# Performance work log

Measured on AMD Instinct MI355X. Metric: run time of the kernel, lower is better.

Reference implementation:

```python
import jax, jax.numpy as jnp
import numpy as np

N, E, IN, H1, H2, C = 50000, 800000, 256, 64, 64, 40
NEG_SLOPE = 0.2


def _glorot(key, shape):
    fan_in = shape[0]
    return jax.random.normal(key, shape, jnp.float32) / np.sqrt(fan_in)


def gat_conv(x, W, al, ar, src, dst, act):
    """DGL-style GATConv (no bias, no residual). al/ar: [H, D]."""
    n = x.shape[0]
    H, D = al.shape
    feat = (x @ W).reshape(n, H, D)                      # [N,H,D]
    el = jnp.sum(feat * al, axis=-1)                     # [N,H]
    er = jnp.sum(feat * ar, axis=-1)                     # [N,H]
    e = jax.nn.leaky_relu(el[src] + er[dst], NEG_SLOPE)  # [E,H]
    # edge softmax over incoming edges of each dst node
    emax = jax.ops.segment_max(e, dst, num_segments=n)
    emax = jnp.where(jnp.isfinite(emax), emax, 0.0)      # guard zero-in-degree
    ex = jnp.exp(e - emax[dst])
    den = jax.ops.segment_sum(ex, dst, num_segments=n)
    alpha = ex / jnp.maximum(den[dst], 1e-9)             # [E,H]
    msg = feat[src] * alpha[..., None]                   # [E,H,D]
    rst = jax.ops.segment_sum(msg, dst, num_segments=n)  # [N,H,D]
    return act(rst) if act is not None else rst


def setup_inputs() -> dict:
    key = jax.random.key(0)
    ks = jax.random.split(key, 24)
    x = jax.random.normal(ks[0], (N, IN), jnp.float32)
    src = jax.random.randint(ks[1], (E,), 0, N, jnp.int32)
    dst = jax.random.randint(ks[2], (E,), 0, N, jnp.int32)
    p = {
        # branch 0 (even): GAT(num_layers=2, heads=[4,1,1])
        "W00": _glorot(ks[3], (IN, 4 * H1)),  "a00l": _glorot(ks[4], (4, H1)),  "a00r": _glorot(ks[5], (4, H1)),
        "W01": _glorot(ks[6], (4 * H1, H1)),  "a01l": _glorot(ks[7], (1, H1)),  "a01r": _glorot(ks[8], (1, H1)),
        "W0f": _glorot(ks[9], (H1, C)),       "a0fl": _glorot(ks[10], (1, C)),  "a0fr": _glorot(ks[11], (1, C)),
        # branch 1 (odd): GAT(num_layers=1, heads=[4,1]) encoder + 1-head output conv
        "W10": _glorot(ks[12], (IN, 4 * H2)), "a10l": _glorot(ks[13], (4, H2)), "a10r": _glorot(ks[14], (4, H2)),
        "W1f": _glorot(ks[15], (4 * H2, H1)), "a1fl": _glorot(ks[16], (1, H1)), "a1fr": _glorot(ks[17], (1, H1)),
        "W1o": _glorot(ks[18], (H1, C)),      "a1ol": _glorot(ks[19], (1, C)),  "a1or": _glorot(ks[20], (1, C)),
    }
    return {"x": x, "src": src, "dst": dst, **p}


def reference(x, src, dst,
              W00, a00l, a00r, W01, a01l, a01r, W0f, a0fl, a0fr,
              W10, a10l, a10r, W1f, a1fl, a1fr, W1o, a1ol, a1or):
    elu = jax.nn.elu
    n = x.shape[0]
    # branch 0: stacked GAT, final layer mean over heads, no activation
    h = gat_conv(x, W00, a00l, a00r, src, dst, elu).reshape(n, -1)   # [N,4*H1]
    h = gat_conv(h, W01, a01l, a01r, src, dst, elu).reshape(n, -1)   # [N,H1]
    y0 = gat_conv(h, W0f, a0fl, a0fr, src, dst, None).mean(axis=1)   # [N,C]
    # branch 1: encoder GAT -> emb, then 1-head output conv with elu
    h = gat_conv(x, W10, a10l, a10r, src, dst, elu).reshape(n, -1)   # [N,4*H2]
    emb = gat_conv(h, W1f, a1fl, a1fr, src, dst, None).mean(axis=1)  # [N,H1]
    y1 = gat_conv(emb, W1o, a1ol, a1or, src, dst, elu)[:, 0, :]      # [N,C]
    return jnp.stack([y0, y1], axis=0)                               # [2,N,C]
```

## Files before the change

### kernel.cpp

```cpp
#include <hip/hip_runtime.h>
#include <math.h>

typedef __attribute__((ext_vector_type(8))) short bf16x8;
typedef __attribute__((ext_vector_type(4))) float f32x4;

#define FMAMIX_LO(acc, pk, s) \
    asm("v_fma_mix_f32 %0, %1, %2, %0 op_sel:[0,0,0] op_sel_hi:[1,0,0]" \
        : "+v"(acc) : "v"(pk), "v"(s))
#define FMAMIX_HI(acc, pk, s) \
    asm("v_fma_mix_f32 %0, %1, %2, %0 op_sel:[1,0,0] op_sel_hi:[1,0,0]" \
        : "+v"(acc) : "v"(pk), "v"(s))

__device__ __forceinline__ unsigned short f2bf(float f) {
    unsigned int u = __float_as_uint(f);
    unsigned int r = (u + 0x7FFF + ((u >> 16) & 1)) >> 16;
    return (unsigned short)r;
}
__device__ __forceinline__ float bf2f(unsigned short h) {
    return __uint_as_float((unsigned int)h << 16);
}
__device__ __forceinline__ void split_bf(float x, unsigned short& hi, unsigned short& lo) {
    hi = f2bf(x);
    lo = f2bf(x - bf2f(hi));
}


__global__ void k_hist(const int* __restrict__ dst, int* __restrict__ deg, int e) {
    int t = blockIdx.x * 256 + threadIdx.x;
    if (t < e) atomicAdd(&deg[dst[t]], 1);
}

__global__ void k_scan1(const int* __restrict__ deg, int* __restrict__ tmp,
                        int* __restrict__ bsum, int n) {
    __shared__ int s[1024];
    int t = threadIdx.x;
    int g = blockIdx.x * 1024 + t;
    int v = (g < n) ? deg[g] : 0;
    s[t] = v;
    __syncthreads();
    for (int off = 1; off < 1024; off <<= 1) {
        int u = (t >= off) ? s[t - off] : 0;
        __syncthreads();
        s[t] += u;
        __syncthreads();
    }
    if (g < n) tmp[g] = s[t];
    if (t == 1023) bsum[blockIdx.x] = s[t];
}

__global__ void k_scan2(int* bsum, int nb) {
    int acc = 0;
    for (int b = 0; b < nb; ++b) { int v = bsum[b]; bsum[b] = acc; acc += v; }
}

__global__ void k_scan3(const int* __restrict__ deg, const int* __restrict__ tmp,
                        const int* __restrict__ bsum, int* __restrict__ rowptr,
                        int* __restrict__ cursor, int n) {
    int g = blockIdx.x * 256 + threadIdx.x;
    if (g < n) {
        int incl = tmp[g] + bsum[g >> 10];
        rowptr[g + 1] = incl;
        cursor[g] = incl - deg[g];
        if (g == 0) rowptr[0] = 0;
    }
}

__global__ void k_scatter(const int* __restrict__ src, const int* __restrict__ dst,
                          int* __restrict__ cursor, int* __restrict__ csr, int e) {
    int t = blockIdx.x * 256 + threadIdx.x;
    if (t < e) {
        int d = dst[t];
        int pos = atomicAdd(&cursor[d], 1);
        csr[pos] = src[t];
    }
}


__global__ void k_castx(const float* __restrict__ x, unsigned short* __restrict__ xhi,
                        unsigned short* __restrict__ xlo, int nvec) {
    int t = blockIdx.x * 256 + threadIdx.x;
    if (t < nvec) {
        float4 v = ((const float4*)x)[t];
        ushort4 h, l;
        split_bf(v.x, h.x, l.x);
        split_bf(v.y, h.y, l.y);
        split_bf(v.z, h.z, l.z);
        split_bf(v.w, h.w, l.w);
        ((ushort4*)xhi)[t] = h;
        ((ushort4*)xlo)[t] = l;
    }
}

struct WSeg { const float* W; unsigned short* Wh; unsigned short* Wl; int K; int N; int cnt; };
__global__ void k_castw_all(WSeg s0, WSeg s1, WSeg s2, WSeg s3, WSeg s4, WSeg s5) {
    int t = blockIdx.x * 256 + threadIdx.x;
    WSeg sg;
    if      (t < s0.cnt) { sg = s0; }
    else if ((t -= s0.cnt) < s1.cnt) { sg = s1; }
    else if ((t -= s1.cnt) < s2.cnt) { sg = s2; }
    else if ((t -= s2.cnt) < s3.cnt) { sg = s3; }
    else if ((t -= s3.cnt) < s4.cnt) { sg = s4; }
    else if ((t -= s4.cnt) < s5.cnt) { sg = s5; }
    else return;
    int k = t / sg.N, n = t - k * sg.N;
    unsigned short h, l;
    split_bf(sg.W[t], h, l);
    sg.Wh[n * sg.K + k] = h;
    sg.Wl[n * sg.K + k] = l;
}


#define LDP 40

__global__ __launch_bounds__(256) void k_gemm_split(const unsigned short* __restrict__ Ahi,
                                                    const unsigned short* __restrict__ Alo,
                                                    const unsigned short* __restrict__ Bhi,
                                                    const unsigned short* __restrict__ Blo,
                                                    _Float16* __restrict__ C,
                                                    int M, int Ncol, int K, int ldc,
                                                    const float* __restrict__ al,
                                                    const float* __restrict__ ar,
                                                    float* __restrict__ el2,
                                                    float* __restrict__ er2, int bsel) {
    int bx = blockIdx.x, by = blockIdx.y;
    __shared__ unsigned short Ash[64 * LDP];
    __shared__ unsigned short Asl[64 * LDP];
    __shared__ unsigned short Bsh[64 * LDP];
    __shared__ unsigned short Bsl[64 * LDP];
    int t = threadIdx.x;
    int w = t >> 6, lane = t & 63;
    int lrow = lane & 15, kgrp = (lane >> 4) * 8;
    int row0 = bx * 64, col0 = by * 64;
    int trow = t >> 2, tcol = (t & 3) * 8;

    f32x4 acc[4] = {{0.f, 0.f, 0.f, 0.f}, {0.f, 0.f, 0.f, 0.f},
                    {0.f, 0.f, 0.f, 0.f}, {0.f, 0.f, 0.f, 0.f}};

    for (int k0 = 0; k0 < K; k0 += 32) {
        uint4 ah = {0u,0u,0u,0u}, al4 = {0u,0u,0u,0u};
        uint4 bh = {0u,0u,0u,0u}, bl4 = {0u,0u,0u,0u};
        int gr = row0 + trow;
        if (gr < M) {
            ah  = *(const uint4*)(Ahi + (size_t)gr * K + k0 + tcol);
            al4 = *(const uint4*)(Alo + (size_t)gr * K + k0 + tcol);
        }
        int gc = col0 + trow;
        if (gc < Ncol) {
            bh  = *(const uint4*)(Bhi + (size_t)gc * K + k0 + tcol);
            bl4 = *(const uint4*)(Blo + (size_t)gc * K + k0 + tcol);
        }
        __syncthreads();
        *(uint4*)&Ash[trow * LDP + tcol] = ah;
        *(uint4*)&Asl[trow * LDP + tcol] = al4;
        *(uint4*)&Bsh[trow * LDP + tcol] = bh;
        *(uint4*)&Bsl[trow * LDP + tcol] = bl4;
        __syncthreads();
        bf16x8 vbh = *(const bf16x8*)&Bsh[(w * 16 + lrow) * LDP + kgrp];
        bf16x8 vbl = *(const bf16x8*)&Bsl[(w * 16 + lrow) * LDP + kgrp];
        #pragma unroll
        for (int mt = 0; mt < 4; ++mt) {
            bf16x8 vah = *(const bf16x8*)&Ash[(mt * 16 + lrow) * LDP + kgrp];
            bf16x8 val = *(const bf16x8*)&Asl[(mt * 16 + lrow) * LDP + kgrp];
            acc[mt] = __builtin_amdgcn_mfma_f32_16x16x32_bf16(vah, vbh, acc[mt], 0, 0, 0);
            acc[mt] = __builtin_amdgcn_mfma_f32_16x16x32_bf16(val, vbh, acc[mt], 0, 0, 0);
            acc[mt] = __builtin_amdgcn_mfma_f32_16x16x32_bf16(vah, vbl, acc[mt], 0, 0, 0);
        }
    }

    int ocol = col0 + w * 16 + lrow;
    int orow = (lane >> 4) * 4;
    if (ocol < Ncol) {
        #pragma unroll
        for (int mt = 0; mt < 4; ++mt) {
            #pragma unroll
            for (int r = 0; r < 4; ++r) {
                int m = row0 + mt * 16 + orow + r;
                if (m < M) C[(size_t)m * ldc + ocol] = (_Float16)acc[mt][r];
            }
        }
    }

    float alv = (ocol < Ncol) ? al[ocol] : 0.f;
    float arv = (ocol < Ncol) ? ar[ocol] : 0.f;
    __syncthreads();
    float* Pl = (float*)Ash;
    float* Pr = (float*)Bsh;
    #pragma unroll
    for (int mt = 0; mt < 4; ++mt) {
        #pragma unroll
        for (int r = 0; r < 4; ++r) {
            float pl = acc[mt][r] * alv;
            float pr = acc[mt][r] * arv;
            #pragma unroll
            for (int off = 1; off < 16; off <<= 1) {
                pl += __shfl_xor(pl, off);
                pr += __shfl_xor(pr, off);
            }
            if (lrow == 0) {
                int rloc = mt * 16 + orow + r;
                Pl[w * 64 + rloc] = pl;
                Pr[w * 64 + rloc] = pr;
            }
        }
    }
    __syncthreads();
    if (t < 64) {
        int m = row0 + t;
        if (m < M) {
            float pl = Pl[t] + Pl[64 + t] + Pl[128 + t] + Pl[192 + t];
            float pr = Pr[t] + Pr[64 + t] + Pr[128 + t] + Pr[192 + t];
            el2[m * 2 + bsel] = pl;
            er2[m * 2 + bsel] = pr;
        }
    }
}

__global__ __launch_bounds__(256) void k_gemm128(const unsigned short* __restrict__ Ahi,
                                                 const unsigned short* __restrict__ Alo,
                                                 const unsigned short* __restrict__ Bhi,
                                                 const unsigned short* __restrict__ Blo,
                                                 _Float16* __restrict__ C,
                                                 int M, int Ncol, int K, int ldc,
                                                 const float* __restrict__ al,
                                                 const float* __restrict__ ar,
                                                 float* __restrict__ el8,
                                                 float* __restrict__ er8, int bsel) {
    int Mb = (M + 127) >> 7;
    int nwg = Mb * 2;
    int v = blockIdx.x;
    int q = nwg >> 3, r = nwg & 7;
    int xcd = v & 7, idx = v >> 3;
    int wg = (xcd < r ? xcd * (q + 1) : r * (q + 1) + (xcd - r) * q) + idx;
    int bx = wg >> 1, by = wg & 1;
    int row0 = bx * 128, col0 = by * 128;

    __shared__ unsigned short Ash[128 * LDP];
    __shared__ unsigned short Asl[128 * LDP];
    __shared__ unsigned short Bsh[128 * LDP];
    __shared__ unsigned short Bsl[128 * LDP];

    int t = threadIdx.x;
    int w = t >> 6, lane = t & 63;
    int wr = w >> 1, wc = w & 1;
    int lrow = lane & 15, kgrp = (lane >> 4) * 8;
    int trow = t >> 1, tcol = (t & 1) * 16;

    f32x4 acc[4][4];
    #pragma unroll
    for (int mt = 0; mt < 4; ++mt)
        #pragma unroll
        for (int nt = 0; nt < 4; ++nt)
            acc[mt][nt] = (f32x4){0.f, 0.f, 0.f, 0.f};

    for (int k0 = 0; k0 < K; k0 += 32) {
        uint4 a0 = {0u,0u,0u,0u}, a1 = {0u,0u,0u,0u};
        uint4 l0 = {0u,0u,0u,0u}, l1 = {0u,0u,0u,0u};
        uint4 b0 = {0u,0u,0u,0u}, b1 = {0u,0u,0u,0u};
        uint4 m0 = {0u,0u,0u,0u}, m1 = {0u,0u,0u,0u};
        int gr = row0 + trow;
        if (gr < M) {
            const unsigned short* pa = Ahi + (size_t)gr * K + k0 + tcol;
            const unsigned short* pl = Alo + (size_t)gr * K + k0 + tcol;
            a0 = *(const uint4*)pa;       a1 = *(const uint4*)(pa + 8);
            l0 = *(const uint4*)pl;       l1 = *(const uint4*)(pl + 8);
        }
        int gc = col0 + trow;
        if (gc < Ncol) {
            const unsigned short* pb = Bhi + (size_t)gc * K + k0 + tcol;
            const unsigned short* pm = Blo + (size_t)gc * K + k0 + tcol;
            b0 = *(const uint4*)pb;       b1 = *(const uint4*)(pb + 8);
            m0 = *(const uint4*)pm;       m1 = *(const uint4*)(pm + 8);
        }
        __syncthreads();
        *(uint4*)&Ash[trow * LDP + tcol]     = a0;
        *(uint4*)&Ash[trow * LDP + tcol + 8] = a1;
        *(uint4*)&Asl[trow * LDP + tcol]     = l0;
        *(uint4*)&Asl[trow * LDP + tcol + 8] = l1;
        *(uint4*)&Bsh[trow * LDP + tcol]     = b0;
        *(uint4*)&Bsh[trow * LDP + tcol + 8] = b1;
        *(uint4*)&Bsl[trow * LDP + tcol]     = m0;
        *(uint4*)&Bsl[trow * LDP + tcol + 8] = m1;
        __syncthreads();

        bf16x8 vbh[4], vbl[4];
        #pragma unroll
        for (int nt = 0; nt < 4; ++nt) {
            vbh[nt] = *(const bf16x8*)&Bsh[(wc * 64 + nt * 16 + lrow) * LDP + kgrp];
            vbl[nt] = *(const bf16x8*)&Bsl[(wc * 64 + nt * 16 + lrow) * LDP + kgrp];
        }
        #pragma unroll
        for (int mt = 0; mt < 4; ++mt) {
            bf16x8 vah = *(const bf16x8*)&Ash[(wr * 64 + mt * 16 + lrow) * LDP + kgrp];
            bf16x8 val = *(const bf16x8*)&Asl[(wr * 64 + mt * 16 + lrow) * LDP + kgrp];
            #pragma unroll
            for (int nt = 0; nt < 4; ++nt) {
                acc[mt][nt] = __builtin_amdgcn_mfma_f32_16x16x32_bf16(vah, vbh[nt], acc[mt][nt], 0, 0, 0);
                acc[mt][nt] = __builtin_amdgcn_mfma_f32_16x16x32_bf16(val, vbh[nt], acc[mt][nt], 0, 0, 0);
                acc[mt][nt] = __builtin_amdgcn_mfma_f32_16x16x32_bf16(vah, vbl[nt], acc[mt][nt], 0, 0, 0);
            }
        }
    }

    int orow = (lane >> 4) * 4;
    #pragma unroll
    for (int mt = 0; mt < 4; ++mt) {
        #pragma unroll
        for (int nt = 0; nt < 4; ++nt) {
            int oc = col0 + wc * 64 + nt * 16 + lrow;
            #pragma unroll
            for (int rr = 0; rr < 4; ++rr) {
                int m = row0 + wr * 64 + mt * 16 + orow + rr;
                if (m < M) C[(size_t)m * ldc + oc] = (_Float16)acc[mt][nt][rr];
            }
        }
    }

    int h = by * 2 + wc;
    float alv[4], arv[4];
    #pragma unroll
    for (int nt = 0; nt < 4; ++nt) {
        int cidx = nt * 16 + lrow;
        alv[nt] = al[h * 64 + cidx];
        arv[nt] = ar[h * 64 + cidx];
    }
    #pragma unroll
    for (int mt = 0; mt < 4; ++mt) {
        #pragma unroll
        for (int rr = 0; rr < 4; ++rr) {
            float pl = 0.f, pr = 0.f;
            #pragma unroll
            for (int nt = 0; nt < 4; ++nt) {
                pl = fmaf(acc[mt][nt][rr], alv[nt], pl);
                pr = fmaf(acc[mt][nt][rr], arv[nt], pr);
            }
            #pragma unroll
            for (int off = 1; off < 16; off <<= 1) {
                pl += __shfl_xor(pl, off);
                pr += __shfl_xor(pr, off);
            }
            int m = row0 + wr * 64 + mt * 16 + orow + rr;
            if (lrow == 0 && m < M) {
                el8[m * 8 + h * 2 + bsel] = pl;
                er8[m * 8 + h * 2 + bsel] = pr;
            }
        }
    }
}

static inline void gemm_split(const unsigned short* Ah, const unsigned short* Al,
                              const unsigned short* Bh, const unsigned short* Bl,
                              _Float16* C, int M, int Ncol, int K, int ldc,
                              const float* al, const float* ar,
                              float* el, float* er, int bsel, hipStream_t st) {
    if (Ncol == 256) {
        int Mb = (M + 127) / 128;
        k_gemm128<<<Mb * 2, 256, 0, st>>>(Ah, Al, Bh, Bl, C, M, Ncol, K, ldc,
                                          al, ar, el, er, bsel);
    } else {
        int Mb = (M + 63) / 64, Nb = (Ncol + 63) / 64;
        k_gemm_split<<<dim3(Mb, Nb), 256, 0, st>>>(Ah, Al, Bh, Bl, C, M, Ncol, K, ldc,
                                                   al, ar, el, er, bsel);
    }
}

__device__ __forceinline__ float lrelu(float v) { return v > 0.f ? v : 0.2f * v; }

#define A42_ISSUE(J) uint4 q##J = *(const uint4*)(featLane + ((size_t)(unsigned)__shfl(s, (J) << 2) << 10))
#define A42_CONS(J, X) \
    FMAMIX_LO(f0, q##J.x, X); FMAMIX_HI(f1, q##J.x, X); \
    FMAMIX_LO(f2, q##J.y, X); FMAMIX_HI(f3, q##J.y, X); \
    FMAMIX_LO(f4, q##J.z, X); FMAMIX_HI(f5, q##J.z, X); \
    FMAMIX_LO(f6, q##J.w, X); FMAMIX_HI(f7, q##J.w, X)

__global__ __launch_bounds__(256) void k_agg4x2(const int* __restrict__ rowptr,
                                                const int* __restrict__ csr,
                                                const float* __restrict__ el8,
                                                const float* __restrict__ er8,
                                                const _Float16* __restrict__ featC,
                                                unsigned short* __restrict__ b0hi,
                                                unsigned short* __restrict__ b0lo,
                                                unsigned short* __restrict__ b1hi,
                                                unsigned short* __restrict__ b1lo,
                                                int n) {
    __shared__ float s_ex[4][128];
    int w = threadIdx.x >> 6;
    int lane = threadIdx.x & 63;
    int i = blockIdx.x * 4 + w;
    if (i >= n) return;
    int s0 = rowptr[i], s1 = rowptr[i + 1];
    int deg = s1 - s0;
    int eidx = lane >> 2, h = lane & 3;
    int b = lane >> 5, hh = (lane >> 3) & 3;
    float2 erp = *(const float2*)&er8[i * 8 + h * 2];
    const char* featLane = (const char*)featC + (lane << 4);

    float den0 = 0.f, den1 = 0.f;
    float m0 = -INFINITY, m1 = -INFINITY;
    float f0 = 0.f, f1 = 0.f, f2 = 0.f, f3 = 0.f;
    float f4 = 0.f, f5 = 0.f, f6 = 0.f, f7 = 0.f;

    int e0 = s0 + eidx;
    int s = (e0 < s1) ? csr[e0] : 0;
    for (int c = s0; c < s1; c += 16) {
        bool val = (c + eidx < s1);
        float2 elp = *(const float2*)&el8[(s << 3) + h * 2];
        A42_ISSUE(0);  A42_ISSUE(1);  A42_ISSUE(2);  A42_ISSUE(3);
        A42_ISSUE(4);  A42_ISSUE(5);  A42_ISSUE(6);  A42_ISSUE(7);
        A42_ISSUE(8);  A42_ISSUE(9);  A42_ISSUE(10); A42_ISSUE(11);
        A42_ISSUE(12); A42_ISSUE(13); A42_ISSUE(14); A42_ISSUE(15);
        int en = c + 16 + eidx;
        int sn = (en < s1) ? csr[en] : 0;
        float v0 = val ? lrelu(elp.x + erp.x) : -INFINITY;
        float v1 = val ? lrelu(elp.y + erp.y) : -INFINITY;
        float cm0 = v0, cm1 = v1;
        #pragma unroll
        for (int off = 4; off < 64; off <<= 1) {
            cm0 = fmaxf(cm0, __shfl_xor(cm0, off));
            cm1 = fmaxf(cm1, __shfl_xor(cm1, off));
        }
        float mn0 = fmaxf(m0, cm0), mn1 = fmaxf(m1, cm1);
        float sc0 = __expf(m0 - mn0), sc1 = __expf(m1 - mn1);
        m0 = mn0; m1 = mn1;
        float ex0 = val ? __expf(v0 - mn0) : 0.f;
        float ex1 = val ? __expf(v1 - mn1) : 0.f;
        den0 = den0 * sc0 + ex0;
        den1 = den1 * sc1 + ex1;
        s_ex[w][(h << 4) + eidx] = ex0;
        s_ex[w][64 + (h << 4) + eidx] = ex1;
        float sb0 = __shfl(sc0, hh), sb1 = __shfl(sc1, hh);
        float scl = (lane < 32) ? sb0 : sb1;
        f0 *= scl; f1 *= scl; f2 *= scl; f3 *= scl;
        f4 *= scl; f5 *= scl; f6 *= scl; f7 *= scl;
        const float* exrow = &s_ex[w][(b << 6) + (hh << 4)];
        float4 x0 = *(const float4*)&exrow[0];
        float4 x1 = *(const float4*)&exrow[4];
        float4 x2 = *(const float4*)&exrow[8];
        float4 x3 = *(const float4*)&exrow[12];
        A42_CONS(0, x0.x);  A42_CONS(1, x0.y);  A42_CONS(2, x0.z);  A42_CONS(3, x0.w);
        A42_CONS(4, x1.x);  A42_CONS(5, x1.y);  A42_CONS(6, x1.z);  A42_CONS(7, x1.w);
        A42_CONS(8, x2.x);  A42_CONS(9, x2.y);  A42_CONS(10, x2.z); A42_CONS(11, x2.w);
        A42_CONS(12, x3.x); A42_CONS(13, x3.y); A42_CONS(14, x3.z); A42_CONS(15, x3.w);
        s = sn;
    }

    #pragma unroll
    for (int off = 4; off < 64; off <<= 1) {
        den0 += __shfl_xor(den0, off);
        den1 += __shfl_xor(den1, off);
    }
    float db0 = __shfl(den0, hh), db1 = __shfl(den1, hh);
    float d = fmaxf((lane < 32) ? db0 : db1, 1e-9f);

    float o0 = (deg > 0) ? f0 / d : 0.f;
    float o1 = (deg > 0) ? f1 / d : 0.f;
    float o2 = (deg > 0) ? f2 / d : 0.f;
    float o3 = (deg > 0) ? f3 / d : 0.f;
    float o4 = (deg > 0) ? f4 / d : 0.f;
    float o5 = (deg > 0) ? f5 / d : 0.f;
    float o6 = (deg > 0) ? f6 / d : 0.f;
    float o7 = (deg > 0) ? f7 / d : 0.f;
    o0 = o0 > 0.f ? o0 : (__expf(o0) - 1.f);
    o1 = o1 > 0.f ? o1 : (__expf(o1) - 1.f);
    o2 = o2 > 0.f ? o2 : (__expf(o2) - 1.f);
    o3 = o3 > 0.f ? o3 : (__expf(o3) - 1.f);
    o4 = o4 > 0.f ? o4 : (__expf(o4) - 1.f);
    o5 = o5 > 0.f ? o5 : (__expf(o5) - 1.f);
    o6 = o6 > 0.f ? o6 : (__expf(o6) - 1.f);
    o7 = o7 > 0.f ? o7 : (__expf(o7) - 1.f);

    ushort4 vhA, vlA, vhB, vlB;
    split_bf(o0, vhA.x, vlA.x);
    split_bf(o1, vhA.y, vlA.y);
    split_bf(o2, vhA.z, vlA.z);
    split_bf(o3, vhA.w, vlA.w);
    split_bf(o4, vhB.x, vlB.x);
    split_bf(o5, vhB.y, vlB.y);
    split_bf(o6, vhB.z, vlB.z);
    split_bf(o7, vhB.w, vlB.w);
    size_t base = (size_t)i * 256 + ((lane & 31) << 3);
    if (lane < 32) {
        *(ushort4*)&b0hi[base] = vhA;  *(ushort4*)&b0hi[base + 4] = vhB;
        *(ushort4*)&b0lo[base] = vlA;  *(ushort4*)&b0lo[base + 4] = vlB;
    } else {
        *(ushort4*)&b1hi[base] = vhA;  *(ushort4*)&b1hi[base + 4] = vhB;
        *(ushort4*)&b1lo[base] = vlA;  *(ushort4*)&b1lo[base + 4] = vlB;
    }
}

template <int DB, int ACT0, int ACT1, int SPLITOUT>
__global__ __launch_bounds__(256) void k_agg1x2(const int* __restrict__ rowptr,
                                                const int* __restrict__ csr,
                                                const float* __restrict__ el2,
                                                const float* __restrict__ er2,
                                                const _Float16* __restrict__ featC,
                                                unsigned short* __restrict__ o0hi,
                                                unsigned short* __restrict__ o0lo,
                                                unsigned short* __restrict__ o1hi,
                                                unsigned short* __restrict__ o1lo,
                                                float* __restrict__ ofp0,
                                                float* __restrict__ ofp1, int n) {
    __shared__ int   s_off[4][64];
    __shared__ float s_ex0[4][64];
    __shared__ float s_ex1[4][64];
    int w = threadIdx.x >> 6;
    int i = blockIdx.x * 4 + w;
    int lane = threadIdx.x & 63;
    if (i >= n) return;
    int s0 = rowptr[i], s1 = rowptr[i + 1];
    int deg = s1 - s0;
    float2 erp = *(const float2*)&er2[i * 2];
    bool act = lane < DB;
    int b = (lane >= (DB / 2)) ? 1 : 0;
    int loc = lane - b * (DB / 2);
    const char* featLane = (const char*)featC + lane * 4;
    const int ROWB = 4 * DB;

    float den0 = 0.f, den1 = 0.f, acc0 = 0.f, acc1 = 0.f;
    float m0 = -INFINITY, m1 = -INFINITY;

    auto fma_chunk = [&](int cnt) {
        const float* exr = b ? s_ex1[w] : s_ex0[w];
        int j = 0;
        for (; j + 4 <= cnt; j += 4) {
            int4   oj = *(const int4*)&s_off[w][j];
            float4 xj = *(const float4*)&exr[j];
            unsigned u0 = act ? *(const unsigned*)(featLane + oj.x) : 0u;
            unsigned u1 = act ? *(const unsigned*)(featLane + oj.y) : 0u;
            unsigned u2 = act ? *(const unsigned*)(featLane + oj.z) : 0u;
            unsigned u3 = act ? *(const unsigned*)(featLane + oj.w) : 0u;
            FMAMIX_LO(acc0, u0, xj.x); FMAMIX_HI(acc1, u0, xj.x);
            FMAMIX_LO(acc0, u1, xj.y); FMAMIX_HI(acc1, u1, xj.y);
            FMAMIX_LO(acc0, u2, xj.z); FMAMIX_HI(acc1, u2, xj.z);
            FMAMIX_LO(acc0, u3, xj.w); FMAMIX_HI(acc1, u3, xj.w);
        }
        for (; j < cnt; ++j) {
            unsigned u0 = act ? *(const unsigned*)(featLane + s_off[w][j]) : 0u;
            float x = exr[j];
            FMAMIX_LO(acc0, u0, x); FMAMIX_HI(acc1, u0, x);
        }
    };

    for (int c = s0; c < s1; c += 64) {
        int e = c + lane;
        bool val = e < s1;
        int s = 0;
        float2 elp = {0.f, 0.f};
        if (val) {
            s = csr[e];
            elp = *(const float2*)&el2[s * 2];
        }
        float v0 = val ? lrelu(elp.x + erp.x) : -INFINITY;
        float v1 = val ? lrelu(elp.y + erp.y) : -INFINITY;
        float cm0 = v0, cm1 = v1;
        #pragma unroll
        for (int off = 32; off; off >>= 1) {
            cm0 = fmaxf(cm0, __shfl_xor(cm0, off));
            cm1 = fmaxf(cm1, __shfl_xor(cm1, off));
        }
        float mn0 = fmaxf(m0, cm0), mn1 = fmaxf(m1, cm1);
        float sc0 = __expf(m0 - mn0), sc1 = __expf(m1 - mn1);
        m0 = mn0; m1 = mn1;
        float ex0 = val ? __expf(v0 - mn0) : 0.f;
        float ex1 = val ? __expf(v1 - mn1) : 0.f;
        den0 = den0 * sc0 + ex0;
        den1 = den1 * sc1 + ex1;
        float scl = b ? sc1 : sc0;
        acc0 *= scl; acc1 *= scl;
        s_off[w][lane] = s * ROWB;
        s_ex0[w][lane] = ex0;
        s_ex1[w][lane] = ex1;
        fma_chunk(min(64, s1 - c));
    }
    #pragma unroll
    for (int off = 32; off; off >>= 1) {
        den0 += __shfl_xor(den0, off);
        den1 += __shfl_xor(den1, off);
    }
    float d = fmaxf(b ? den1 : den0, 1e-9f);

    float o0 = (deg > 0) ? acc0 / d : 0.f;
    float o1 = (deg > 0) ? acc1 / d : 0.f;
    int actflag = b ? ACT1 : ACT0;
    if (actflag) {
        o0 = o0 > 0.f ? o0 : (__expf(o0) - 1.f);
        o1 = o1 > 0.f ? o1 : (__expf(o1) - 1.f);
    }
    if (act) {
        if (SPLITOUT) {
            unsigned short h0, l0, h1, l1;
            split_bf(o0, h0, l0);
            split_bf(o1, h1, l1);
            ushort2 vh = {h0, h1}, vl = {l0, l1};
            if (b == 0) {
                *(ushort2*)&o0hi[(size_t)i * DB + 2 * loc] = vh;
                *(ushort2*)&o0lo[(size_t)i * DB + 2 * loc] = vl;
            } else {
                *(ushort2*)&o1hi[(size_t)i * DB + 2 * loc] = vh;
                *(ushort2*)&o1lo[(size_t)i * DB + 2 * loc] = vl;
            }
        } else {
            float2 vo = {o0, o1};
            if (b == 0) *(float2*)&ofp0[(size_t)i * DB + 2 * loc] = vo;
            else        *(float2*)&ofp1[(size_t)i * DB + 2 * loc] = vo;
        }
    }
}


extern "C" void kernel_launch(void* const* d_in, const int* in_sizes, int n_in,
                              void* d_out, int out_size, void* d_ws, size_t ws_size,
                              hipStream_t stream) {
    const float* x    = (const float*)d_in[0];
    const int*   src  = (const int*)d_in[1];
    const int*   dst  = (const int*)d_in[2];
    const float* W00  = (const float*)d_in[3];
    const float* a00l = (const float*)d_in[4];
    const float* a00r = (const float*)d_in[5];
    const float* W01  = (const float*)d_in[6];
    const float* a01l = (const float*)d_in[7];
    const float* a01r = (const float*)d_in[8];
    const float* W0f  = (const float*)d_in[9];
    const float* a0fl = (const float*)d_in[10];
    const float* a0fr = (const float*)d_in[11];
    const float* W10  = (const float*)d_in[12];
    const float* a10l = (const float*)d_in[13];
    const float* a10r = (const float*)d_in[14];
    const float* W1f  = (const float*)d_in[15];
    const float* a1fl = (const float*)d_in[16];
    const float* a1fr = (const float*)d_in[17];
    const float* W1o  = (const float*)d_in[18];
    const float* a1ol = (const float*)d_in[19];
    const float* a1or = (const float*)d_in[20];
    float* out = (float*)d_out;

    const int n = in_sizes[0] / 256;
    const int e = in_sizes[1];
    const int C = 40;

    char* p = (char*)d_ws;
    auto alloc = [&](size_t bytes) -> void* {
        void* r = (void*)p;
        p += (bytes + 255) & ~(size_t)255;
        return r;
    };
    int*   deg     = (int*)alloc((size_t)n * 4);
    int*   tmp     = (int*)alloc((size_t)n * 4);
    int*   bsum    = (int*)alloc(64 * 4);
    int*   rowptr  = (int*)alloc((size_t)(n + 1) * 4);
    int*   cursor  = (int*)alloc((size_t)n * 4);
    int*   csr     = (int*)alloc((size_t)e * 4);
    float* el8     = (float*)alloc((size_t)n * 8 * 4);
    float* er8     = (float*)alloc((size_t)n * 8 * 4);
    _Float16* featC = (_Float16*)alloc((size_t)n * 512 * 2 + 256);
    unsigned short* xhi = (unsigned short*)alloc((size_t)n * 256 * 2);
    unsigned short* xlo = (unsigned short*)alloc((size_t)n * 256 * 2);
    unsigned short* hhi = (unsigned short*)alloc((size_t)n * 256 * 2);
    unsigned short* hlo = (unsigned short*)alloc((size_t)n * 256 * 2);
    unsigned short* W00h = (unsigned short*)alloc(256 * 256 * 2);
    unsigned short* W00l = (unsigned short*)alloc(256 * 256 * 2);
    unsigned short* W01h = (unsigned short*)alloc(256 * 64 * 2);
    unsigned short* W01l = (unsigned short*)alloc(256 * 64 * 2);
    unsigned short* W0fh = (unsigned short*)alloc(64 * 40 * 2);
    unsigned short* W0fl = (unsigned short*)alloc(64 * 40 * 2);
    unsigned short* W10h = (unsigned short*)alloc(256 * 256 * 2);
    unsigned short* W10l = (unsigned short*)alloc(256 * 256 * 2);
    unsigned short* W1fh = (unsigned short*)alloc(256 * 64 * 2);
    unsigned short* W1fl = (unsigned short*)alloc(256 * 64 * 2);
    unsigned short* W1oh = (unsigned short*)alloc(64 * 40 * 2);
    unsigned short* W1ol = (unsigned short*)alloc(64 * 40 * 2);

    hipMemsetAsync(deg, 0, (size_t)n * 4, stream);
    k_hist<<<(e + 255) / 256, 256, 0, stream>>>(dst, deg, e);
    int nb = (n + 1023) / 1024;
    k_scan1<<<nb, 1024, 0, stream>>>(deg, tmp, bsum, n);
    k_scan2<<<1, 1, 0, stream>>>(bsum, nb);
    k_scan3<<<(n + 255) / 256, 256, 0, stream>>>(deg, tmp, bsum, rowptr, cursor, n);
    k_scatter<<<(e + 255) / 256, 256, 0, stream>>>(src, dst, cursor, csr, e);

    int nel = n * 256;
    k_castx<<<(nel / 4 + 255) / 256, 256, 0, stream>>>(x, xhi, xlo, nel / 4);
    {
        WSeg s0 = {W00, W00h, W00l, 256, 256, 256 * 256};
        WSeg s1 = {W10, W10h, W10l, 256, 256, 256 * 256};
        WSeg s2 = {W01, W01h, W01l, 256, 64, 256 * 64};
        WSeg s3 = {W1f, W1fh, W1fl, 256, 64, 256 * 64};
        WSeg s4 = {W0f, W0fh, W0fl, 64, 40, 64 * 40};
        WSeg s5 = {W1o, W1oh, W1ol, 64, 40, 64 * 40};
        int tot = 2 * 65536 + 2 * 16384 + 2 * 2560;
        k_castw_all<<<(tot + 255) / 256, 256, 0, stream>>>(s0, s1, s2, s3, s4, s5);
    }

    int gw1 = (n + 3) / 4;

    gemm_split(xhi, xlo, W00h, W00l, featC,       n, 256, 256, 512,
               a00l, a00r, el8, er8, 0, stream);
    gemm_split(xhi, xlo, W10h, W10l, featC + 256, n, 256, 256, 512,
               a10l, a10r, el8, er8, 1, stream);
    k_agg4x2<<<gw1, 256, 0, stream>>>(rowptr, csr, el8, er8, featC, hhi, hlo, xhi, xlo, n);

    gemm_split(hhi, hlo, W01h, W01l, featC,      n, 64, 256, 128,
               a01l, a01r, el8, er8, 0, stream);
    gemm_split(xhi, xlo, W1fh, W1fl, featC + 64, n, 64, 256, 128,
               a1fl, a1fr, el8, er8, 1, stream);
    k_agg1x2<64, 1, 0, 1><<<gw1, 256, 0, stream>>>(rowptr, csr, el8, er8, featC,
                                                   hhi, hlo, xhi, xlo, nullptr, nullptr, n);

    gemm_split(hhi, hlo, W0fh, W0fl, featC,      n, C, 64, 80,
               a0fl, a0fr, el8, er8, 0, stream);
    gemm_split(xhi, xlo, W1oh, W1ol, featC + 40, n, C, 64, 80,
               a1ol, a1or, el8, er8, 1, stream);
    k_agg1x2<40, 0, 1, 0><<<gw1, 256, 0, stream>>>(rowptr, csr, el8, er8, featC,
                                                   nullptr, nullptr, nullptr, nullptr,
                                                   out, out + (size_t)n * C, n);
}
```

Baseline: 583.6 us.

## Fuse x bf16 split into first GEMM, batch branch GEMMs, parallelize scan2

The first-layer GEMM now reads fp32 x directly and splits it into bf16 hi/lo inside the load loop, which removes the separate cast kernel and its write and re-read of xhi/xlo. Both branches' first-layer GEMMs are launched as one grid, and the later paired GEMMs run in a single launch via blockIdx.y, cutting launch count. The serial single-thread block-sum scan is replaced by a 64-lane wavefront shuffle scan. The trade-off is that x is converted twice, once per branch/column tile, adding ALU work and extra fp32 reads in the GEMM. The scan rewrite assumes nb ≤ 64, which holds here (50000/1024 gives 49).

Result: faster. 535.5 us (-8.2%).

```diff
diff --git a/kernel.cpp b/kernel.cpp
--- a/kernel.cpp
+++ b/kernel.cpp
@@ -49,8 +49,15 @@
 }
 
 __global__ void k_scan2(int* bsum, int nb) {
-    int acc = 0;
-    for (int b = 0; b < nb; ++b) { int v = bsum[b]; bsum[b] = acc; acc += v; }
+    int lane = threadIdx.x;
+    int orig = (lane < nb) ? bsum[lane] : 0;
+    int v = orig;
+    #pragma unroll
+    for (int off = 1; off < 64; off <<= 1) {
+        int u = __shfl_up(v, off);
+        if (lane >= off) v += u;
+    }
+    if (lane < nb) bsum[lane] = v - orig;
 }
 
 __global__ void k_scan3(const int* __restrict__ deg, const int* __restrict__ tmp,
@@ -75,21 +82,6 @@
     }
 }
 
-
-__global__ void k_castx(const float* __restrict__ x, unsigned short* __restrict__ xhi,
-                        unsigned short* __restrict__ xlo, int nvec) {
-    int t = blockIdx.x * 256 + threadIdx.x;
-    if (t < nvec) {
-        float4 v = ((const float4*)x)[t];
-        ushort4 h, l;
-        split_bf(v.x, h.x, l.x);
-        split_bf(v.y, h.y, l.y);
-        split_bf(v.z, h.z, l.z);
-        split_bf(v.w, h.w, l.w);
-        ((ushort4*)xhi)[t] = h;
-        ((ushort4*)xlo)[t] = l;
-    }
-}
 
 struct WSeg { const float* W; unsigned short* Wh; unsigned short* Wl; int K; int N; int cnt; };
 __global__ void k_castw_all(WSeg s0, WSeg s1, WSeg s2, WSeg s3, WSeg s4, WSeg s5) {
@@ -109,20 +101,193 @@
     sg.Wl[n * sg.K + k] = l;
 }
 
-
 #define LDP 40
 
-__global__ __launch_bounds__(256) void k_gemm_split(const unsigned short* __restrict__ Ahi,
-                                                    const unsigned short* __restrict__ Alo,
-                                                    const unsigned short* __restrict__ Bhi,
-                                                    const unsigned short* __restrict__ Blo,
-                                                    _Float16* __restrict__ C,
-                                                    int M, int Ncol, int K, int ldc,
-                                                    const float* __restrict__ al,
-                                                    const float* __restrict__ ar,
-                                                    float* __restrict__ el2,
-                                                    float* __restrict__ er2, int bsel) {
-    int bx = blockIdx.x, by = blockIdx.y;
+__global__ __launch_bounds__(256) void k_gemm128f(const float* __restrict__ X,
+                                                  const unsigned short* __restrict__ B0h,
+                                                  const unsigned short* __restrict__ B0l,
+                                                  const unsigned short* __restrict__ B1h,
+                                                  const unsigned short* __restrict__ B1l,
+                                                  _Float16* __restrict__ C,
+                                                  int M, int K,
+                                                  const float* __restrict__ a0l,
+                                                  const float* __restrict__ a0r,
+                                                  const float* __restrict__ a1l,
+                                                  const float* __restrict__ a1r,
+                                                  float* __restrict__ el8,
+                                                  float* __restrict__ er8) {
+    int Mb = (M + 127) >> 7;
+    int nwg = Mb * 2;
+    int v = blockIdx.x;
+    int bsel = (v >= nwg) ? 1 : 0;
+    v -= bsel * nwg;
+    int q = nwg >> 3, r = nwg & 7;
+    int xcd = v & 7, idx = v >> 3;
+    int wg = (xcd < r ? xcd * (q + 1) : r * (q + 1) + (xcd - r) * q) + idx;
+    int bx = wg >> 1, by = wg & 1;
+    int row0 = bx * 128, col0 = by * 128;
+    const unsigned short* Bh = bsel ? B1h : B0h;
+    const unsigned short* Bl = bsel ? B1l : B0l;
+    const float* alp = bsel ? a1l : a0l;
+    const float* arp = bsel ? a1r : a0r;
+    _Float16* Cb = C + bsel * 256;
+
+    __shared__ unsigned short Ash[128 * LDP];
+    __shared__ unsigned short Asl[128 * LDP];
+    __shared__ unsigned short Bsh[128 * LDP];
+    __shared__ unsigned short Bsl[128 * LDP];
+
+    int t = threadIdx.x;
+    int w = t >> 6, lane = t & 63;
+    int wr = w >> 1, wc = w & 1;
+    int lrow = lane & 15, kgrp = (lane >> 4) * 8;
+    int trow = t >> 1, tcol = (t & 1) * 16;
+
+    f32x4 acc[4][4];
+    #pragma unroll
+    for (int mt = 0; mt < 4; ++mt)
+        #pragma unroll
+        for (int nt = 0; nt < 4; ++nt)
+            acc[mt][nt] = (f32x4){0.f, 0.f, 0.f, 0.f};
+
+    for (int k0 = 0; k0 < K; k0 += 32) {
+        uint4 ah0 = {0u,0u,0u,0u}, ah1 = {0u,0u,0u,0u};
+        uint4 av0 = {0u,0u,0u,0u}, av1 = {0u,0u,0u,0u};
+        uint4 b0 = {0u,0u,0u,0u}, b1 = {0u,0u,0u,0u};
+        uint4 m0 = {0u,0u,0u,0u}, m1 = {0u,0u,0u,0u};
+        int gr = row0 + trow;
+        if (gr < M) {
+            const float* px = X + (size_t)gr * K + k0 + tcol;
+            float4 f0 = *(const float4*)px;
+            float4 f1 = *(const float4*)(px + 4);
+            float4 f2 = *(const float4*)(px + 8);
+            float4 f3 = *(const float4*)(px + 12);
+            float ff[16] = {f0.x, f0.y, f0.z, f0.w, f1.x, f1.y, f1.z, f1.w,
+                            f2.x, f2.y, f2.z, f2.w, f3.x, f3.y, f3.z, f3.w};
+            unsigned hp[8], lp[8];
+            #pragma unroll
+            for (int j = 0; j < 8; ++j) {
+                unsigned short ha, la, hb, lb;
+                split_bf(ff[2 * j], ha, la);
+                split_bf(ff[2 * j + 1], hb, lb);
+                hp[j] = (unsigned)ha | ((unsigned)hb << 16);
+                lp[j] = (unsigned)la | ((unsigned)lb << 16);
+            }
+            ah0 = (uint4){hp[0], hp[1], hp[2], hp[3]};
+            ah1 = (uint4){hp[4], hp[5], hp[6], hp[7]};
+            av0 = (uint4){lp[0], lp[1], lp[2], lp[3]};
+            av1 = (uint4){lp[4], lp[5], lp[6], lp[7]};
+        }
+        int gc = col0 + trow;
+        {
+            const unsigned short* pb = Bh + (size_t)gc * K + k0 + tcol;
+            const unsigned short* pm = Bl + (size_t)gc * K + k0 + tcol;
+            b0 = *(const uint4*)pb;       b1 = *(const uint4*)(pb + 8);
+            m0 = *(const uint4*)pm;       m1 = *(const uint4*)(pm + 8);
+        }
+        __syncthreads();
+        *(uint4*)&Ash[trow * LDP + tcol]     = ah0;
+        *(uint4*)&Ash[trow * LDP + tcol + 8] = ah1;
+        *(uint4*)&Asl[trow * LDP + tcol]     = av0;
+        *(uint4*)&Asl[trow * LDP + tcol + 8] = av1;
+        *(uint4*)&Bsh[trow * LDP + tcol]     = b0;
+        *(uint4*)&Bsh[trow * LDP + tcol + 8] = b1;
+        *(uint4*)&Bsl[trow * LDP + tcol]     = m0;
+        *(uint4*)&Bsl[trow * LDP + tcol + 8] = m1;
+        __syncthreads();
+
+        bf16x8 vbh[4], vbl[4];
+        #pragma unroll
+        for (int nt = 0; nt < 4; ++nt) {
+            vbh[nt] = *(const bf16x8*)&Bsh[(wc * 64 + nt * 16 + lrow) * LDP + kgrp];
+            vbl[nt] = *(const bf16x8*)&Bsl[(wc * 64 + nt * 16 + lrow) * LDP + kgrp];
+        }
+        #pragma unroll
+        for (int mt = 0; mt < 4; ++mt) {
+            bf16x8 vah = *(const bf16x8*)&Ash[(wr * 64 + mt * 16 + lrow) * LDP + kgrp];
+            bf16x8 val = *(const bf16x8*)&Asl[(wr * 64 + mt * 16 + lrow) * LDP + kgrp];
+            #pragma unroll
+            for (int nt = 0; nt < 4; ++nt) {
+                acc[mt][nt] = __builtin_amdgcn_mfma_f32_16x16x32_bf16(vah, vbh[nt], acc[mt][nt], 0, 0, 0);
+                acc[mt][nt] = __builtin_amdgcn_mfma_f32_16x16x32_bf16(val, vbh[nt], acc[mt][nt], 0, 0, 0);
+                acc[mt][nt] = __builtin_amdgcn_mfma_f32_16x16x32_bf16(vah, vbl[nt], acc[mt][nt], 0, 0, 0);
+            }
+        }
+    }
+
+    int orow = (lane >> 4) * 4;
+    #pragma unroll
+    for (int mt = 0; mt < 4; ++mt) {
+        #pragma unroll
+        for (int nt = 0; nt < 4; ++nt) {
+            int oc = col0 + wc * 64 + nt * 16 + lrow;
+            #pragma unroll
+            for (int rr = 0; rr < 4; ++rr) {
+                int m = row0 + wr * 64 + mt * 16 + orow + rr;
+                if (m < M) Cb[(size_t)m * 512 + oc] = (_Float16)acc[mt][nt][rr];
+            }
+        }
+    }
+
+    int h = by * 2 + wc;
+    float alv[4], arv[4];
+    #pragma unroll
+    for (int nt = 0; nt < 4; ++nt) {
+        int cidx = nt * 16 + lrow;
+        alv[nt] = alp[h * 64 + cidx];
+        arv[nt] = arp[h * 64 + cidx];
+    }
+    #pragma unroll
+    for (int mt = 0; mt < 4; ++mt) {
+        #pragma unroll
+        for (int rr = 0; rr < 4; ++rr) {
+            float pl = 0.f, pr = 0.f;
+            #pragma unroll
+            for (int nt = 0; nt < 4; ++nt) {
+                pl = fmaf(acc[mt][nt][rr], alv[nt], pl);
+                pr = fmaf(acc[mt][nt][rr], arv[nt], pr);
+            }
+            #pragma unroll
+            for (int off = 1; off < 16; off <<= 1) {
+                pl += __shfl_xor(pl, off);
+                pr += __shfl_xor(pr, off);
+            }
+            int m = row0 + wr * 64 + mt * 16 + orow + rr;
+            if (lrow == 0 && m < M) {
+                el8[m * 8 + h * 2 + bsel] = pl;
+                er8[m * 8 + h * 2 + bsel] = pr;
+            }
+        }
+    }
+}
+
+__global__ __launch_bounds__(256) void k_gemm_split2(const unsigned short* __restrict__ A0hi,
+                                                     const unsigned short* __restrict__ A0lo,
+                                                     const unsigned short* __restrict__ B0hp,
+                                                     const unsigned short* __restrict__ B0lp,
+                                                     const unsigned short* __restrict__ A1hi,
+                                                     const unsigned short* __restrict__ A1lo,
+                                                     const unsigned short* __restrict__ B1hp,
+                                                     const unsigned short* __restrict__ B1lp,
+                                                     _Float16* __restrict__ C0,
+                                                     _Float16* __restrict__ C1,
+                                                     int M, int Ncol, int K, int ldc,
+                                                     const float* __restrict__ a0lp,
+                                                     const float* __restrict__ a0rp,
+                                                     const float* __restrict__ a1lp,
+                                                     const float* __restrict__ a1rp,
+                                                     float* __restrict__ el2,
+                                                     float* __restrict__ er2) {
+    int bx = blockIdx.x;
+    int bsel = blockIdx.y;
+    const unsigned short* Ahi = bsel ? A1hi : A0hi;
+    const unsigned short* Alo = bsel ? A1lo : A0lo;
+    const unsigned short* Bhi = bsel ? B1hp : B0hp;
+    const unsigned short* Blo = bsel ? B1lp : B0lp;
+    const float* al = bsel ? a1lp : a0lp;
+    const float* ar = bsel ? a1rp : a0rp;
+    _Float16* C = bsel ? C1 : C0;
+
     __shared__ unsigned short Ash[64 * LDP];
     __shared__ unsigned short Asl[64 * LDP];
     __shared__ unsigned short Bsh[64 * LDP];
@@ -130,7 +295,7 @@
     int t = threadIdx.x;
     int w = t >> 6, lane = t & 63;
     int lrow = lane & 15, kgrp = (lane >> 4) * 8;
-    int row0 = bx * 64, col0 = by * 64;
+    int row0 = bx * 64;
     int trow = t >> 2, tcol = (t & 3) * 8;
 
     f32x4 acc[4] = {{0.f, 0.f, 0.f, 0.f}, {0.f, 0.f, 0.f, 0.f},
@@ -144,10 +309,9 @@
             ah  = *(const uint4*)(Ahi + (size_t)gr * K + k0 + tcol);
             al4 = *(const uint4*)(Alo + (size_t)gr * K + k0 + tcol);
         }
-        int gc = col0 + trow;
-        if (gc < Ncol) {
-            bh  = *(const uint4*)(Bhi + (size_t)gc * K + k0 + tcol);
-            bl4 = *(const uint4*)(Blo + (size_t)gc * K + k0 + tcol);
+        if (trow < Ncol) {
+            bh  = *(const uint4*)(Bhi + (size_t)trow * K + k0 + tcol);
+            bl4 = *(const uint4*)(Blo + (size_t)trow * K + k0 + tcol);
         }
         __syncthreads();
         *(uint4*)&Ash[trow * LDP + tcol] = ah;
@@ -167,7 +331,7 @@
         }
     }
 
-    int ocol = col0 + w * 16 + lrow;
+    int ocol = w * 16 + lrow;
     int orow = (lane >> 4) * 4;
     if (ocol < Ncol) {
         #pragma unroll
@@ -212,154 +376,6 @@
             el2[m * 2 + bsel] = pl;
             er2[m * 2 + bsel] = pr;
         }
-    }
-}
-
-__global__ __launch_bounds__(256) void k_gemm128(const unsigned short* __restrict__ Ahi,
-                                                 const unsigned short* __restrict__ Alo,
-                                                 const unsigned short* __restrict__ Bhi,
-                                                 const unsigned short* __restrict__ Blo,
-                                                 _Float16* __restrict__ C,
-                                                 int M, int Ncol, int K, int ldc,
-                                                 const float* __restrict__ al,
-                                                 const float* __restrict__ ar,
-                                                 float* __restrict__ el8,
-                                                 float* __restrict__ er8, int bsel) {
-    int Mb = (M + 127) >> 7;
-    int nwg = Mb * 2;
-    int v = blockIdx.x;
-    int q = nwg >> 3, r = nwg & 7;
-    int xcd = v & 7, idx = v >> 3;
-    int wg = (xcd < r ? xcd * (q + 1) : r * (q + 1) + (xcd - r) * q) + idx;
-    int bx = wg >> 1, by = wg & 1;
-    int row0 = bx * 128, col0 = by * 128;
-
-    __shared__ unsigned short Ash[128 * LDP];
-    __shared__ unsigned short Asl[128 * LDP];
-    __shared__ unsigned short Bsh[128 * LDP];
-    __shared__ unsigned short Bsl[128 * LDP];
-
-    int t = threadIdx.x;
-    int w = t >> 6, lane = t & 63;
-    int wr = w >> 1, wc = w & 1;
-    int lrow = lane & 15, kgrp = (lane >> 4) * 8;
-    int trow = t >> 1, tcol = (t & 1) * 16;
-
-    f32x4 acc[4][4];
-    #pragma unroll
-    for (int mt = 0; mt < 4; ++mt)
-        #pragma unroll
-        for (int nt = 0; nt < 4; ++nt)
-            acc[mt][nt] = (f32x4){0.f, 0.f, 0.f, 0.f};
-
-    for (int k0 = 0; k0 < K; k0 += 32) {
-        uint4 a0 = {0u,0u,0u,0u}, a1 = {0u,0u,0u,0u};
-        uint4 l0 = {0u,0u,0u,0u}, l1 = {0u,0u,0u,0u};
-        uint4 b0 = {0u,0u,0u,0u}, b1 = {0u,0u,0u,0u};
-        uint4 m0 = {0u,0u,0u,0u}, m1 = {0u,0u,0u,0u};
-        int gr = row0 + trow;
-        if (gr < M) {
-            const unsigned short* pa = Ahi + (size_t)gr * K + k0 + tcol;
-            const unsigned short* pl = Alo + (size_t)gr * K + k0 + tcol;
-            a0 = *(const uint4*)pa;       a1 = *(const uint4*)(pa + 8);
-            l0 = *(const uint4*)pl;       l1 = *(const uint4*)(pl + 8);
-        }
-        int gc = col0 + trow;
-        if (gc < Ncol) {
-            const unsigned short* pb = Bhi + (size_t)gc * K + k0 + tcol;
-            const unsigned short* pm = Blo + (size_t)gc * K + k0 + tcol;
-            b0 = *(const uint4*)pb;       b1 = *(const uint4*)(pb + 8);
-            m0 = *(const uint4*)pm;       m1 = *(const uint4*)(pm + 8);
-        }
-        __syncthreads();
-        *(uint4*)&Ash[trow * LDP + tcol]     = a0;
-        *(uint4*)&Ash[trow * LDP + tcol + 8] = a1;
-        *(uint4*)&Asl[trow * LDP + tcol]     = l0;
-        *(uint4*)&Asl[trow * LDP + tcol + 8] = l1;
-        *(uint4*)&Bsh[trow * LDP + tcol]     = b0;
-        *(uint4*)&Bsh[trow * LDP + tcol + 8] = b1;
-        *(uint4*)&Bsl[trow * LDP + tcol]     = m0;
-        *(uint4*)&Bsl[trow * LDP + tcol + 8] = m1;
-        __syncthreads();
-
-        bf16x8 vbh[4], vbl[4];
-        #pragma unroll
-        for (int nt = 0; nt < 4; ++nt) {
-            vbh[nt] = *(const bf16x8*)&Bsh[(wc * 64 + nt * 16 + lrow) * LDP + kgrp];
-            vbl[nt] = *(const bf16x8*)&Bsl[(wc * 64 + nt * 16 + lrow) * LDP + kgrp];
-        }
-        #pragma unroll
-        for (int mt = 0; mt < 4; ++mt) {
-            bf16x8 vah = *(const bf16x8*)&Ash[(wr * 64 + mt * 16 + lrow) * LDP + kgrp];
-            bf16x8 val = *(const bf16x8*)&Asl[(wr * 64 + mt * 16 + lrow) * LDP + kgrp];
-            #pragma unroll
-            for (int nt = 0; nt < 4; ++nt) {
-                acc[mt][nt] = __builtin_amdgcn_mfma_f32_16x16x32_bf16(vah, vbh[nt], acc[mt][nt], 0, 0, 0);
-                acc[mt][nt] = __builtin_amdgcn_mfma_f32_16x16x32_bf16(val, vbh[nt], acc[mt][nt], 0, 0, 0);
-                acc[mt][nt] = __builtin_amdgcn_mfma_f32_16x16x32_bf16(vah, vbl[nt], acc[mt][nt], 0, 0, 0);
-            }
-        }
-    }
-
-    int orow = (lane >> 4) * 4;
-    #pragma unroll
-    for (int mt = 0; mt < 4; ++mt) {
-        #pragma unroll
-        for (int nt = 0; nt < 4; ++nt) {
-            int oc = col0 + wc * 64 + nt * 16 + lrow;
-            #pragma unroll
-            for (int rr = 0; rr < 4; ++rr) {
-                int m = row0 + wr * 64 + mt * 16 + orow + rr;
-                if (m < M) C[(size_t)m * ldc + oc] = (_Float16)acc[mt][nt][rr];
-            }
-        }
-    }
-
-    int h = by * 2 + wc;
-    float alv[4], arv[4];
-    #pragma unroll
-    for (int nt = 0; nt < 4; ++nt) {
-        int cidx = nt * 16 + lrow;
-        alv[nt] = al[h * 64 + cidx];
-        arv[nt] = ar[h * 64 + cidx];
-    }
-    #pragma unroll
-    for (int mt = 0; mt < 4; ++mt) {
-        #pragma unroll
-        for (int rr = 0; rr < 4; ++rr) {
-            float pl = 0.f, pr = 0.f;
-            #pragma unroll
-            for (int nt = 0; nt < 4; ++nt) {
-                pl = fmaf(acc[mt][nt][rr], alv[nt], pl);
-                pr = fmaf(acc[mt][nt][rr], arv[nt], pr);
-            }
-            #pragma unroll
-            for (int off = 1; off < 16; off <<= 1) {
-                pl += __shfl_xor(pl, off);
-                pr += __shfl_xor(pr, off);
-            }
-            int m = row0 + wr * 64 + mt * 16 + orow + rr;
-            if (lrow == 0 && m < M) {
-                el8[m * 8 + h * 2 + bsel] = pl;
-                er8[m * 8 + h * 2 + bsel] = pr;
-            }
-        }
-    }
-}
-
-static inline void gemm_split(const unsigned short* Ah, const unsigned short* Al,
-                              const unsigned short* Bh, const unsigned short* Bl,
-                              _Float16* C, int M, int Ncol, int K, int ldc,
-                              const float* al, const float* ar,
-                              float* el, float* er, int bsel, hipStream_t st) {
-    if (Ncol == 256) {
-        int Mb = (M + 127) / 128;
-        k_gemm128<<<Mb * 2, 256, 0, st>>>(Ah, Al, Bh, Bl, C, M, Ncol, K, ldc,
-                                          al, ar, el, er, bsel);
-    } else {
-        int Mb = (M + 63) / 64, Nb = (Ncol + 63) / 64;
-        k_gemm_split<<<dim3(Mb, Nb), 256, 0, st>>>(Ah, Al, Bh, Bl, C, M, Ncol, K, ldc,
-                                                   al, ar, el, er, bsel);
     }
 }
 
@@ -673,12 +689,10 @@
     k_hist<<<(e + 255) / 256, 256, 0, stream>>>(dst, deg, e);
     int nb = (n + 1023) / 1024;
     k_scan1<<<nb, 1024, 0, stream>>>(deg, tmp, bsum, n);
-    k_scan2<<<1, 1, 0, stream>>>(bsum, nb);
+    k_scan2<<<1, 64, 0, stream>>>(bsum, nb);
     k_scan3<<<(n + 255) / 256, 256, 0, stream>>>(deg, tmp, bsum, rowptr, cursor, n);
     k_scatter<<<(e + 255) / 256, 256, 0, stream>>>(src, dst, cursor, csr, e);
 
-    int nel = n * 256;
-    k_castx<<<(nel / 4 + 255) / 256, 256, 0, stream>>>(x, xhi, xlo, nel / 4);
     {
         WSeg s0 = {W00, W00h, W00l, 256, 256, 256 * 256};
         WSeg s1 = {W10, W10h, W10l, 256, 256, 256 * 256};
@@ -691,24 +705,32 @@
     }
 
     int gw1 = (n + 3) / 4;
-
-    gemm_split(xhi, xlo, W00h, W00l, featC,       n, 256, 256, 512,
-               a00l, a00r, el8, er8, 0, stream);
-    gemm_split(xhi, xlo, W10h, W10l, featC + 256, n, 256, 256, 512,
-               a10l, a10r, el8, er8, 1, stream);
+    int Mb128 = (n + 127) / 128;
+
+    k_gemm128f<<<Mb128 * 2 * 2, 256, 0, stream>>>(x, W00h, W00l, W10h, W10l, featC,
+                                                  n, 256, a00l, a00r, a10l, a10r,
+                                                  el8, er8);
     k_agg4x2<<<gw1, 256, 0, stream>>>(rowptr, csr, el8, er8, featC, hhi, hlo, xhi, xlo, n);
 
-    gemm_split(hhi, hlo, W01h, W01l, featC,      n, 64, 256, 128,
-               a01l, a01r, el8, er8, 0, stream);
-    gemm_split(xhi, xlo, W1fh, W1fl, featC + 64, n, 64, 256, 128,
-               a1fl, a1fr, el8, er8, 1, stream);
+    {
+        dim3 g((n + 63) / 64, 2);
+        k_gemm_split2<<<g, 256, 0, stream>>>(hhi, hlo, W01h, W01l,
+                                             xhi, xlo, W1fh, W1fl,
+                                             featC, featC + 64,
+                                             n, 64, 256, 128,
+                                             a01l, a01r, a1fl, a1fr, el8, er8);
+    }
     k_agg1x2<64, 1, 0, 1><<<gw1, 256, 0, stream>>>(rowptr, csr, el8, er8, featC,
                                                    hhi, hlo, xhi, xlo, nullptr, nullptr, n);
 
-    gemm_split(hhi, hlo, W0fh, W0fl, featC,      n, C, 64, 80,
-               a0fl, a0fr, el8, er8, 0, stream);
-    gemm_split(xhi, xlo, W1oh, W1ol, featC + 40, n, C, 64, 80,
-               a1ol, a1or, el8, er8, 1, stream);
+    {
+        dim3 g((n + 63) / 64, 2);
+        k_gemm_split2<<<g, 256, 0, stream>>>(hhi, hlo, W0fh, W0fl,
+                                             xhi, xlo, W1oh, W1ol,
+                                             featC, featC + 40,
+                                             n, C, 64, 80,
+                                             a0fl, a0fr, a1ol, a1or, el8, er8);
+    }
     k_agg1x2<40, 0, 1, 0><<<gw1, 256, 0, stream>>>(rowptr, csr, el8, er8, featC,
                                                    nullptr, nullptr, nullptr, nullptr,
                                                    out, out + (size_t)n * C, n);
```
